# Kernel tuning notes

Hardware: AMD Instinct MI355X
Metric: run time of the kernel (lower is better)

The kernel has to match this reference:

```python
import jax, jax.numpy as jnp
import numpy as np

B, T, D, H = 2, 4096, 768, 12
HD = D // H  # head_dim = 64


def setup_inputs() -> dict:
    key = jax.random.key(0)
    ks = jax.random.split(key, 6)
    s = 0.02
    return {
        "x": jax.random.normal(ks[0], (B, T, D), dtype=jnp.float32),
        "Wq": jax.random.normal(ks[1], (D, D), dtype=jnp.float32) * s,
        "Wk": jax.random.normal(ks[2], (D, D), dtype=jnp.float32) * s,
        "Wv": jax.random.normal(ks[3], (D, D), dtype=jnp.float32) * s,
        "Wo": jax.random.normal(ks[4], (D, D), dtype=jnp.float32) * s,
        "bo": jnp.zeros((D,), dtype=jnp.float32),
    }


def reference(x, Wq, Wk, Wv, Wo, bo):
    b, t, d = x.shape
    # QKV projections (no bias), reshape to [B, H, T, HD]
    def heads(w):
        return (x @ w.T).reshape(b, t, H, HD).transpose(0, 2, 1, 3)
    q, k, v = heads(Wq), heads(Wk), heads(Wv)
    scores = jnp.einsum("bhqd,bhkd->bhqk", q, k)  # [B,H,T,T]
    causal = jnp.tril(jnp.ones((t, t), dtype=bool))
    scores = jnp.where(causal, scores, -jnp.inf)
    attn = jax.nn.softmax(scores / jnp.sqrt(jnp.float32(HD)), axis=-1)
    ctx = jnp.einsum("bhqk,bhkd->bhqd", attn, v)  # [B,H,T,HD]
    ctx = ctx.transpose(0, 2, 1, 3).reshape(b, t, d)
    return ctx @ Wo.T + bo
```

## Files before the change

### kernel.cpp

```cpp
#include <hip/hip_runtime.h>
#include <hip/hip_bf16.h>
#include <cstdint>
#include <cstddef>

#define B_  2
#define T_  4096
#define D_  768
#define H_  12
#define HD_ 64
#define M_  (B_*T_)

#define SCL 0.18033688f

typedef __bf16 bf16x8 __attribute__((ext_vector_type(8)));
typedef float  f32x4  __attribute__((ext_vector_type(4)));
using bf16 = __hip_bfloat16;

__device__ inline float fexp2(float x) {
  float r; asm("v_exp_f32 %0, %1" : "=v"(r) : "v"(x)); return r;
}
__device__ inline uint32_t fu(float x) { union { float f; uint32_t u; } c; c.f = x; return c.u; }
__device__ inline uint32_t pktr(float a, float b) {
  return __builtin_amdgcn_perm(fu(b), fu(a), 0x07060302);
}
#define GLD16(g, l) __builtin_amdgcn_global_load_lds( \
    (const __attribute__((address_space(1))) uint32_t*)(const void*)(g), \
    (__attribute__((address_space(3))) uint32_t*)(void*)(l), 16, 0, 0)

__global__ void cvt_all(const float* __restrict__ x,
                        const float* __restrict__ w0, const float* __restrict__ w1,
                        const float* __restrict__ w2, const float* __restrict__ w3,
                        bf16* __restrict__ xd,
                        bf16* __restrict__ d0, bf16* __restrict__ d1,
                        bf16* __restrict__ d2, bf16* __restrict__ d3) {
  int blk = blockIdx.x;
  const float* s; bf16* d; int i;
  if (blk < 6144) {
    s = x; d = xd; i = blk * 256 + threadIdx.x;
  } else {
    int q = blk - 6144, which = q / 576, rb = q % 576;
    switch (which) {
      case 0: s = w0; d = d0; break;
      case 1: s = w1; d = d1; break;
      case 2: s = w2; d = d2; break;
      default: s = w3; d = d3; break;
    }
    i = rb * 256 + threadIdx.x;
  }
  float4 v = ((const float4*)s)[i];
  union { bf16 o[4]; uint2 u; } pk;
  pk.o[0] = __float2bfloat16(v.x); pk.o[1] = __float2bfloat16(v.y);
  pk.o[2] = __float2bfloat16(v.z); pk.o[3] = __float2bfloat16(v.w);
  *(uint2*)(d + 4 * (size_t)i) = pk.u;
}

__global__ __launch_bounds__(256) void gemm_qkv(const bf16* __restrict__ x,
                                                const bf16* __restrict__ W0,
                                                const bf16* __restrict__ W1,
                                                const bf16* __restrict__ W2,
                                                bf16* __restrict__ O0,
                                                bf16* __restrict__ O1,
                                                bf16* __restrict__ O2t) {
  __shared__ bf16 As[2][4096];
  __shared__ bf16 Bs[2][4096];
  const int flat = blockIdx.x;
  const int by = flat / 18;
  const int rr = flat % 18;
  const int z  = rr / 6;
  const int bx = rr % 6;
  const bf16* Wz = (z == 0) ? W0 : ((z == 1) ? W1 : W2);
  const char* Ap; const char* Bp; int a0, b0;
  if (z == 2) { Ap = (const char*)x;  a0 = by * 128; Bp = (const char*)Wz; b0 = bx * 128; }
  else        { Ap = (const char*)Wz; a0 = bx * 128; Bp = (const char*)x;  b0 = by * 128; }
  const int t = threadIdx.x;
  const int w = t >> 6, lane = t & 63;
  const int wa = (w >> 1) * 64, wb = (w & 1) * 64;
  const int mi = lane & 15, qd = lane >> 4;

  int aoff[2], boff[2];
  #pragma unroll
  for (int i = 0; i < 2; ++i) {
    int L = i * 256 + t;
    int row = L >> 2, sl = L & 3, c = sl ^ (row & 3);
    aoff[i] = (a0 + row) * 1536 + c * 16;
    boff[i] = (b0 + row) * 1536 + c * 16;
  }
  const int fsw = (qd ^ (mi & 3)) * 8;

  f32x4 acc[4][4] = {};

  #pragma unroll
  for (int i = 0; i < 2; ++i) {
    GLD16(Ap + aoff[i], &As[0][i * 2048 + w * 512]);
    GLD16(Bp + boff[i], &Bs[0][i * 2048 + w * 512]);
  }

  for (int kk = 0; kk < 24; ++kk) {
    __syncthreads();
    const int par = kk & 1;
    if (kk + 1 < 24) {
      const int np = par ^ 1, kb = (kk + 1) * 64;
      #pragma unroll
      for (int i = 0; i < 2; ++i) {
        GLD16(Ap + aoff[i] + kb, &As[np][i * 2048 + w * 512]);
        GLD16(Bp + boff[i] + kb, &Bs[np][i * 2048 + w * 512]);
      }
    }
    bf16x8 af[4], bfr[4];
    #pragma unroll
    for (int at = 0; at < 4; ++at)
      af[at] = *(const bf16x8*)&As[par][(wa + at * 16 + mi) * 32 + fsw];
    #pragma unroll
    for (int bt = 0; bt < 4; ++bt)
      bfr[bt] = *(const bf16x8*)&Bs[par][(wb + bt * 16 + mi) * 32 + fsw];
    #pragma unroll
    for (int at = 0; at < 4; ++at)
      #pragma unroll
      for (int bt = 0; bt < 4; ++bt)
        acc[at][bt] = __builtin_amdgcn_mfma_f32_16x16x32_bf16(af[at], bfr[bt], acc[at][bt], 0, 0, 0);
  }

  if (z == 2) {
    #pragma unroll
    for (int at = 0; at < 4; ++at)
      #pragma unroll
      for (int bt = 0; bt < 4; ++bt) {
        int gr = a0 + wa + at * 16 + qd * 4;
        int gc = b0 + wb + bt * 16 + mi;
        union { bf16 o[4]; uint2 u; } pk;
        #pragma unroll
        for (int r = 0; r < 4; ++r) pk.o[r] = __float2bfloat16(acc[at][bt][r]);
        int bb = gr >> 12, tt = gr & 4095;
        *(uint2*)(O2t + (size_t)bb * 768 * 4096 + (size_t)gc * 4096 + tt) = pk.u;
      }
  } else {
    const float scl = (z == 1) ? SCL : 1.0f;
    bf16* Ob = (z == 0) ? O0 : O1;
    #pragma unroll
    for (int at = 0; at < 4; ++at)
      #pragma unroll
      for (int bt = 0; bt < 4; ++bt) {
        int f0  = a0 + wa + at * 16 + qd * 4;
        int tkn = b0 + wb + bt * 16 + mi;
        union { bf16 o[4]; uint2 u; } pk;
        #pragma unroll
        for (int r = 0; r < 4; ++r) pk.o[r] = __float2bfloat16(acc[at][bt][r] * scl);
        *(uint2*)(Ob + (size_t)tkn * 768 + f0) = pk.u;
      }
  }
}

__global__ __launch_bounds__(256) void gemm_out(const bf16* __restrict__ ctx,
                                                const bf16* __restrict__ Wo,
                                                float* __restrict__ Cf,
                                                const float* __restrict__ bias) {
  __shared__ bf16 As[2][2048];
  __shared__ bf16 Bs[2][4096];
  const int flat = blockIdx.x;
  const int by = flat / 12, bx = flat % 12;
  const char* Ap = (const char*)Wo;  const int a0 = bx * 64;
  const char* Bp = (const char*)ctx; const int b0 = by * 128;
  const int t = threadIdx.x;
  const int w = t >> 6, lane = t & 63;
  const int wa = (w >> 1) * 32, wb = (w & 1) * 64;
  const int mi = lane & 15, qd = lane >> 4;

  int aoff, boff[2];
  { int row = t >> 2, sl = t & 3, c = sl ^ (row & 3);
    aoff = (a0 + row) * 1536 + c * 16; }
  #pragma unroll
  for (int i = 0; i < 2; ++i) {
    int L = i * 256 + t;
    int row = L >> 2, sl = L & 3, c = sl ^ (row & 3);
    boff[i] = (b0 + row) * 1536 + c * 16;
  }
  const int fsw = (qd ^ (mi & 3)) * 8;

  f32x4 acc[2][4] = {};

  GLD16(Ap + aoff, &As[0][w * 512]);
  #pragma unroll
  for (int i = 0; i < 2; ++i)
    GLD16(Bp + boff[i], &Bs[0][i * 2048 + w * 512]);

  for (int kk = 0; kk < 24; ++kk) {
    __syncthreads();
    const int par = kk & 1;
    if (kk + 1 < 24) {
      const int np = par ^ 1, kb = (kk + 1) * 64;
      GLD16(Ap + aoff + kb, &As[np][w * 512]);
      #pragma unroll
      for (int i = 0; i < 2; ++i)
        GLD16(Bp + boff[i] + kb, &Bs[np][i * 2048 + w * 512]);
    }
    bf16x8 af[2], bfr[4];
    #pragma unroll
    for (int at = 0; at < 2; ++at)
      af[at] = *(const bf16x8*)&As[par][(wa + at * 16 + mi) * 32 + fsw];
    #pragma unroll
    for (int bt = 0; bt < 4; ++bt)
      bfr[bt] = *(const bf16x8*)&Bs[par][(wb + bt * 16 + mi) * 32 + fsw];
    #pragma unroll
    for (int at = 0; at < 2; ++at)
      #pragma unroll
      for (int bt = 0; bt < 4; ++bt)
        acc[at][bt] = __builtin_amdgcn_mfma_f32_16x16x32_bf16(af[at], bfr[bt], acc[at][bt], 0, 0, 0);
  }

  #pragma unroll
  for (int at = 0; at < 2; ++at)
    #pragma unroll
    for (int bt = 0; bt < 4; ++bt) {
      int f0  = a0 + wa + at * 16 + qd * 4;
      int tkn = b0 + wb + bt * 16 + mi;
      float4 bv = *(const float4*)&bias[f0];
      float4 o;
      o.x = acc[at][bt][0] + bv.x; o.y = acc[at][bt][1] + bv.y;
      o.z = acc[at][bt][2] + bv.z; o.w = acc[at][bt][3] + bv.w;
      *(float4*)&Cf[(size_t)tkn * 768 + f0] = o;
    }
}

__global__ __launch_bounds__(256, 5) void flash_attn(const bf16* __restrict__ Q,
                                                     const bf16* __restrict__ K,
                                                     const bf16* __restrict__ Vt,
                                                     bf16* __restrict__ ctx) {
  __shared__ bf16 Ks[2][4096];
  __shared__ bf16 Vs[2][4096];
  const int t = threadIdx.x;
  const int w = t >> 6, lane = t & 63;
  const int mi = lane & 15, qd = lane >> 4;
  const int bh   = blockIdx.x % 24;
  const int qrev = blockIdx.x / 24;
  const int q0 = T_ - 64 - qrev * 64;
  const int b = bh / H_, h = bh % H_;
  const size_t bTD = (size_t)b * T_ * D_;
  const char* Kp = (const char*)(K  + bTD + (size_t)h * HD_);
  const char* Vp = (const char*)(Vt + (size_t)b * D_ * T_ + (size_t)h * HD_ * T_);
  const int qw = q0 + w * 16;

  int vkoff[2], vvoff[2];
  #pragma unroll
  for (int i = 0; i < 2; ++i) {
    int L = i * 256 + t;
    int rl = L >> 3, c = (L & 7) ^ (rl & 7);
    int jrow = (rl & 32) | ((rl & 0xC) << 1) | ((rl & 16) >> 2) | (rl & 3);
    vkoff[i] = jrow * 1536 + c * 16;
    vvoff[i] = rl * 8192 + c * 16;
  }

  int fidx[4][2];
  #pragma unroll
  for (int jt = 0; jt < 4; ++jt)
    #pragma unroll
    for (int kt = 0; kt < 2; ++kt)
      fidx[jt][kt] = (jt * 16 + mi) * 64 + (((kt * 4 + qd) ^ (mi & 7)) * 8);

  bf16x8 qf[2];
  const bf16* Qp = Q + bTD + (size_t)h * HD_;
  #pragma unroll
  for (int kt = 0; kt < 2; ++kt)
    qf[kt] = *(const bf16x8*)(Qp + (size_t)(qw + mi) * D_ + kt * 32 + qd * 8);

  f32x4 oacc[4] = {};
  float lst = 0.f;
  const int ntiles = q0 / 64 + 1;

  #pragma unroll
  for (int i = 0; i < 2; ++i) {
    GLD16(Kp + vkoff[i], &Ks[0][i * 2048 + w * 512]);
    GLD16(Vp + vvoff[i], &Vs[0][i * 2048 + w * 512]);
  }

  for (int tt = 0; tt < ntiles; ++tt) {
    __syncthreads();
    const int par = tt & 1;
    if (tt + 1 < ntiles) {
      const size_t j1 = (size_t)(tt + 1) * 64;
      const int np = par ^ 1;
      #pragma unroll
      for (int i = 0; i < 2; ++i) {
        GLD16(Kp + vkoff[i] + j1 * 1536, &Ks[np][i * 2048 + w * 512]);
        GLD16(Vp + vvoff[i] + j1 * 2,    &Vs[np][i * 2048 + w * 512]);
      }
    }
    const int j0 = tt * 64;
    if (j0 > qw + 15) continue;

    f32x4 sacc[4] = {};
    __builtin_amdgcn_s_setprio(1);
    #pragma unroll
    for (int jt = 0; jt < 4; ++jt)
      #pragma unroll
      for (int kt = 0; kt < 2; ++kt) {
        bf16x8 kf = *(const bf16x8*)&Ks[par][fidx[jt][kt]];
        sacc[jt] = __builtin_amdgcn_mfma_f32_16x16x32_bf16(kf, qf[kt], sacc[jt], 0, 0, 0);
      }
    __builtin_amdgcn_s_setprio(0);

    if (j0 + 63 > qw) {
      const int qg = qw + mi;
      #pragma unroll
      for (int jt = 0; jt < 4; ++jt)
        #pragma unroll
        for (int r = 0; r < 4; ++r) {
          int jg = j0 + ((jt >> 1) << 5) + (qd << 3) + ((jt & 1) << 2) + r;
          if (jg > qg) sacc[jt][r] = -1e30f;
        }
    }

    uint32_t pu[4][2];
    #pragma unroll
    for (int jt = 0; jt < 4; ++jt) {
      float p0 = fexp2(sacc[jt][0]);
      float p1 = fexp2(sacc[jt][1]);
      float p2 = fexp2(sacc[jt][2]);
      float p3 = fexp2(sacc[jt][3]);
      lst += (p0 + p1) + (p2 + p3);
      pu[jt][0] = pktr(p0, p1);
      pu[jt][1] = pktr(p2, p3);
    }
    bf16x8 pB[2];
    #pragma unroll
    for (int kt = 0; kt < 2; ++kt) {
      union { uint32_t u[4]; bf16x8 v; } m;
      m.u[0] = pu[2 * kt][0];     m.u[1] = pu[2 * kt][1];
      m.u[2] = pu[2 * kt + 1][0]; m.u[3] = pu[2 * kt + 1][1];
      pB[kt] = m.v;
    }

    __builtin_amdgcn_s_setprio(1);
    #pragma unroll
    for (int kt = 0; kt < 2; ++kt)
      #pragma unroll
      for (int dt = 0; dt < 4; ++dt) {
        bf16x8 vf = *(const bf16x8*)&Vs[par][fidx[dt][kt]];
        oacc[dt] = __builtin_amdgcn_mfma_f32_16x16x32_bf16(vf, pB[kt], oacc[dt], 0, 0, 0);
      }
    __builtin_amdgcn_s_setprio(0);
  }

  float l = lst;
  l += __shfl_xor(l, 16);
  l += __shfl_xor(l, 32);
  float inv = __builtin_amdgcn_rcpf(l);
  const int qg = qw + mi;
  bf16* cp = ctx + bTD + (size_t)qg * D_ + h * HD_ + qd * 4;
  #pragma unroll
  for (int dt = 0; dt < 4; ++dt) {
    union { bf16 o[4]; uint2 u; } pko;
    #pragma unroll
    for (int r = 0; r < 4; ++r) pko.o[r] = __float2bfloat16(oacc[dt][r] * inv);
    *(uint2*)(cp + dt * 16) = pko.u;
  }
}

extern "C" void kernel_launch(void* const* d_in, const int* in_sizes, int n_in,
                              void* d_out, int out_size, void* d_ws, size_t ws_size,
                              hipStream_t stream) {
  const float* x  = (const float*)d_in[0];
  const float* Wq = (const float*)d_in[1];
  const float* Wk = (const float*)d_in[2];
  const float* Wv = (const float*)d_in[3];
  const float* Wo = (const float*)d_in[4];
  const float* bo = (const float*)d_in[5];
  float* out = (float*)d_out;

  char* ws = (char*)d_ws;
  const size_t SZ  = (size_t)M_ * D_ * 2;
  const size_t WSZ = (size_t)D_ * D_ * 2;
  bf16* xb   = (bf16*)(ws);
  bf16* Qb   = (bf16*)(ws + 1 * SZ);
  bf16* Kb   = (bf16*)(ws + 2 * SZ);
  bf16* Vtg  = (bf16*)(ws + 3 * SZ);
  bf16* ctxb = (bf16*)(ws + 4 * SZ);
  bf16* Wqb  = (bf16*)(ws + 5 * SZ);
  bf16* Wkb  = (bf16*)(ws + 5 * SZ + 1 * WSZ);
  bf16* Wvb  = (bf16*)(ws + 5 * SZ + 2 * WSZ);
  bf16* Wob  = (bf16*)(ws + 5 * SZ + 3 * WSZ);

  cvt_all<<<6144 + 4 * 576, 256, 0, stream>>>(x, Wq, Wk, Wv, Wo, xb, Wqb, Wkb, Wvb, Wob);

  gemm_qkv<<<1152, 256, 0, stream>>>(xb, Wqb, Wkb, Wvb, Qb, Kb, Vtg);

  flash_attn<<<(T_ / 64) * B_ * H_, 256, 0, stream>>>(Qb, Kb, Vtg, ctxb);

  gemm_out<<<768, 256, 0, stream>>>(ctxb, Wob, out, bo);
}
```

Baseline: 234.1 us.

## Triple-buffer shared-memory tiles in QKV and output projection GEMMs

Both projection GEMMs move from double to triple buffering of the LDS A/B tiles, prefetching two k-steps ahead. The full __syncthreads is replaced by an explicit s_waitcnt vmcnt on outstanding global-to-LDS loads plus a raw s_barrier, so more load latency can overlap with MFMA work. This costs 50% more shared memory per block, which may reduce occupancy. It also depends on the vmcnt counts exactly matching the number of in-flight GLD16s per stage.

```diff
diff --git a/kernel.cpp b/kernel.cpp
--- a/kernel.cpp
+++ b/kernel.cpp
@@ -61,8 +61,8 @@
                                                 bf16* __restrict__ O0,
                                                 bf16* __restrict__ O1,
                                                 bf16* __restrict__ O2t) {
-  __shared__ bf16 As[2][4096];
-  __shared__ bf16 Bs[2][4096];
+  __shared__ bf16 As[3][4096];
+  __shared__ bf16 Bs[3][4096];
   const int flat = blockIdx.x;
   const int by = flat / 18;
   const int rr = flat % 18;
@@ -90,29 +90,34 @@
   f32x4 acc[4][4] = {};
 
   #pragma unroll
-  for (int i = 0; i < 2; ++i) {
-    GLD16(Ap + aoff[i], &As[0][i * 2048 + w * 512]);
-    GLD16(Bp + boff[i], &Bs[0][i * 2048 + w * 512]);
-  }
-
+  for (int p = 0; p < 2; ++p)
+    #pragma unroll
+    for (int i = 0; i < 2; ++i) {
+      GLD16(Ap + aoff[i] + p * 64, &As[p][i * 2048 + w * 512]);
+      GLD16(Bp + boff[i] + p * 64, &Bs[p][i * 2048 + w * 512]);
+    }
+
+  #pragma unroll 3
   for (int kk = 0; kk < 24; ++kk) {
-    __syncthreads();
-    const int par = kk & 1;
-    if (kk + 1 < 24) {
-      const int np = par ^ 1, kb = (kk + 1) * 64;
+    const int cur = kk % 3;
+    if (kk < 23) asm volatile("s_waitcnt vmcnt(4)" ::: "memory");
+    else         asm volatile("s_waitcnt vmcnt(0)" ::: "memory");
+    __builtin_amdgcn_s_barrier();
+    if (kk + 2 < 24) {
+      const int nb = (kk + 2) % 3, kb = (kk + 2) * 64;
       #pragma unroll
       for (int i = 0; i < 2; ++i) {
-        GLD16(Ap + aoff[i] + kb, &As[np][i * 2048 + w * 512]);
-        GLD16(Bp + boff[i] + kb, &Bs[np][i * 2048 + w * 512]);
+        GLD16(Ap + aoff[i] + kb, &As[nb][i * 2048 + w * 512]);
+        GLD16(Bp + boff[i] + kb, &Bs[nb][i * 2048 + w * 512]);
       }
     }
     bf16x8 af[4], bfr[4];
     #pragma unroll
     for (int at = 0; at < 4; ++at)
-      af[at] = *(const bf16x8*)&As[par][(wa + at * 16 + mi) * 32 + fsw];
+      af[at] = *(const bf16x8*)&As[cur][(wa + at * 16 + mi) * 32 + fsw];
     #pragma unroll
     for (int bt = 0; bt < 4; ++bt)
-      bfr[bt] = *(const bf16x8*)&Bs[par][(wb + bt * 16 + mi) * 32 + fsw];
+      bfr[bt] = *(const bf16x8*)&Bs[cur][(wb + bt * 16 + mi) * 32 + fsw];
     #pragma unroll
     for (int at = 0; at < 4; ++at)
       #pragma unroll
@@ -154,8 +159,8 @@
                                                 const bf16* __restrict__ Wo,
                                                 float* __restrict__ Cf,
                                                 const float* __restrict__ bias) {
-  __shared__ bf16 As[2][2048];
-  __shared__ bf16 Bs[2][4096];
+  __shared__ bf16 As[3][2048];
+  __shared__ bf16 Bs[3][4096];
   const int flat = blockIdx.x;
   const int by = flat / 12, bx = flat % 12;
   const char* Ap = (const char*)Wo;  const int a0 = bx * 64;
@@ -178,28 +183,34 @@
 
   f32x4 acc[2][4] = {};
 
-  GLD16(Ap + aoff, &As[0][w * 512]);
-  #pragma unroll
-  for (int i = 0; i < 2; ++i)
-    GLD16(Bp + boff[i], &Bs[0][i * 2048 + w * 512]);
-
+  #pragma unroll
+  for (int p = 0; p < 2; ++p) {
+    GLD16(Ap + aoff + p * 64, &As[p][w * 512]);
+    #pragma unroll
+    for (int i = 0; i < 2; ++i)
+      GLD16(Bp + boff[i] + p * 64, &Bs[p][i * 2048 + w * 512]);
+  }
+
+  #pragma unroll 3
   for (int kk = 0; kk < 24; ++kk) {
-    __syncthreads();
-    const int par = kk & 1;
-    if (kk + 1 < 24) {
-      const int np = par ^ 1, kb = (kk + 1) * 64;
-      GLD16(Ap + aoff + kb, &As[np][w * 512]);
+    const int cur = kk % 3;
+    if (kk < 23) asm volatile("s_waitcnt vmcnt(3)" ::: "memory");
+    else         asm volatile("s_waitcnt vmcnt(0)" ::: "memory");
+    __builtin_amdgcn_s_barrier();
+    if (kk + 2 < 24) {
+      const int nb = (kk + 2) % 3, kb = (kk + 2) * 64;
+      GLD16(Ap + aoff + kb, &As[nb][w * 512]);
       #pragma unroll
       for (int i = 0; i < 2; ++i)
-        GLD16(Bp + boff[i] + kb, &Bs[np][i * 2048 + w * 512]);
+        GLD16(Bp + boff[i] + kb, &Bs[nb][i * 2048 + w * 512]);
     }
     bf16x8 af[2], bfr[4];
     #pragma unroll
     for (int at = 0; at < 2; ++at)
-      af[at] = *(const bf16x8*)&As[par][(wa + at * 16 + mi) * 32 + fsw];
+      af[at] = *(const bf16x8*)&As[cur][(wa + at * 16 + mi) * 32 + fsw];
     #pragma unroll
     for (int bt = 0; bt < 4; ++bt)
-      bfr[bt] = *(const bf16x8*)&Bs[par][(wb + bt * 16 + mi) * 32 + fsw];
+      bfr[bt] = *(const bf16x8*)&Bs[cur][(wb + bt * 16 + mi) * 32 + fsw];
     #pragma unroll
     for (int at = 0; at < 2; ++at)
       #pragma unroll
```

New measurement: 243.7 us. +4.1%, slower.
